# Optimization experiments

Hardware: AMD Instinct MI355X
Metric: run time of the kernel (lower is better)

## Reference

```python
import jax, jax.numpy as jnp
import numpy as np

N_NODES = 50000


def _sage_conv(x, src, dst, W_l, b_l, W_r, n_nodes):
    # mean-aggregate neighbor (source) features onto targets
    msg = x[src]                                   # [E, d_in] gather
    agg = jax.ops.segment_sum(msg, dst, num_segments=n_nodes)   # [N, d_in]
    deg = jax.ops.segment_sum(jnp.ones((src.shape[0],), x.dtype), dst,
                              num_segments=n_nodes)
    agg = agg / jnp.clip(deg, 1.0, None)[:, None]  # mean with deg>=1 clamp (PyG)
    # out = lin_l(agg) + lin_r(x)   (bias lives in lin_l)
    return agg @ W_l.T + b_l + x @ W_r.T


def setup_inputs() -> dict:
    key = jax.random.key(0)
    ks = jax.random.split(key, 8)
    d_in, d_hid, d_out = 128, 256, 128
    n_edges = 800000
    x = jax.random.normal(ks[0], (N_NODES, d_in), dtype=jnp.float32)
    edge_index = jax.random.randint(ks[1], (2, n_edges), 0, N_NODES, dtype=jnp.int32)
    def glorot(k, shape):
        lim = float(np.sqrt(6.0 / (shape[0] + shape[1])))
        return jax.random.uniform(k, shape, jnp.float32, -lim, lim)
    return {
        "x": x,
        "edge_index": edge_index,
        "W1l": glorot(ks[2], (d_hid, d_in)),
        "b1": jnp.zeros((d_hid,), jnp.float32),
        "W1r": glorot(ks[3], (d_hid, d_in)),
        "W2l": glorot(ks[4], (d_out, d_hid)),
        "b2": jnp.zeros((d_out,), jnp.float32),
        "W2r": glorot(ks[5], (d_out, d_hid)),
    }


def reference(x, edge_index, W1l, b1, W1r, W2l, b2, W2r):
    src, dst = edge_index[0], edge_index[1]
    h = jax.nn.relu(_sage_conv(x, src, dst, W1l, b1, W1r, N_NODES))
    out = _sage_conv(h, src, dst, W2l, b2, W2r, N_NODES)
    return out
```

## Files before the change

kernel.cpp:

```cpp
#include <hip/hip_runtime.h>
#include <hip/hip_bf16.h>

#define NN 50000
#define NN_PAD 50176
#define NE 800000
#define NB 196
#define CAP 6144
#define EPB 4096

typedef __attribute__((ext_vector_type(8))) short short8;
typedef __attribute__((ext_vector_type(4))) float f32x4;

__device__ __forceinline__ unsigned short f2bf(float f) {
    union { float f; unsigned u; } v; v.f = f;
    unsigned u = v.u;
    return (unsigned short)((u + 0x7fffu + ((u >> 16) & 1u)) >> 16);
}
__device__ __forceinline__ float bfu_lo(unsigned u) {
    union { unsigned u; float f; } v; v.u = u << 16; return v.f;
}
__device__ __forceinline__ float bfu_hi(unsigned u) {
    union { unsigned u; float f; } v; v.u = u & 0xffff0000u; return v.f;
}

__global__ void k_setup(const float* __restrict__ W1l, const float* __restrict__ W1r,
                        const float* __restrict__ W2l, const float* __restrict__ W2r,
                        unsigned short* __restrict__ W1pk, unsigned short* __restrict__ W2pk,
                        const float4* __restrict__ x4, unsigned short* __restrict__ x_bf,
                        int* __restrict__ gcursor) {
    int blk = blockIdx.x, t = threadIdx.x;
    if (blk < 64) {
        int tid = blk * 256 + t;
        int table = tid >> 13;
        int r = tid & 8191;
        int lane = r & 63, ni = (r >> 6) & 3, ks = (r >> 8) & 7, g = r >> 11;
        int lm = lane & 15, lq = lane >> 4;
        int o = g * 64 + ni * 16 + lm;
        int k = ks * 32 + lq * 8;
        unsigned short v[8];
        if (table == 0) {
            if (k < 128) {
#pragma unroll
                for (int j = 0; j < 8; ++j) v[j] = f2bf(W1l[o * 128 + k + j]);
            } else {
#pragma unroll
                for (int j = 0; j < 8; ++j) v[j] = f2bf(W1r[o * 128 + k - 128 + j]);
            }
            *(uint4*)(W1pk + (size_t)r * 8) = *(const uint4*)v;
        } else {
            if (o < 128) {
#pragma unroll
                for (int j = 0; j < 8; ++j) v[j] = f2bf(W2l[o * 256 + k + j]);
            } else {
#pragma unroll
                for (int j = 0; j < 8; ++j) v[j] = f2bf(W2r[(o - 128) * 256 + k + j]);
            }
            *(uint4*)(W2pk + (size_t)r * 8) = *(const uint4*)v;
        }
    } else if (blk < 6314) {
        int gid = (blk - 64) * 256 + t;
        int n = gid >> 5, c = gid & 31;
        float4 v = x4[(size_t)n * 32 + c];
        ushort4 o;
        o.x = f2bf(v.x); o.y = f2bf(v.y); o.z = f2bf(v.z); o.w = f2bf(v.w);
        *(ushort4*)(x_bf + (size_t)n * 128 + c * 4) = o;
    } else {
        gcursor[t] = t * CAP;
    }
}

__global__ void k_part(const int* __restrict__ src, const int* __restrict__ dst,
                       int* __restrict__ gcursor, unsigned* __restrict__ pairs) {
    __shared__ int cnt[256];
    __shared__ int base[256];
    int t = threadIdx.x;
    cnt[t] = 0;
    __syncthreads();
    int e0 = blockIdx.x * EPB;
    int eend = min(e0 + EPB, NE);
    int rank[16], bk[16];
    unsigned pk[16];
    int m = 0;
    for (int e = e0 + t; e < eend; e += 256) {
        int s = src[e], d = dst[e];
        bk[m] = d >> 8;
        pk[m] = ((unsigned)s << 8) | (unsigned)(d & 255);
        rank[m] = atomicAdd(&cnt[bk[m]], 1);
        ++m;
    }
    __syncthreads();
    if (t < NB && cnt[t] > 0) base[t] = atomicAdd(&gcursor[t], cnt[t]);
    __syncthreads();
    for (int i = 0; i < m; ++i) {
        int pos = base[bk[i]] + rank[i];
        if (pos < (bk[i] + 1) * CAP) pairs[pos] = pk[i];
    }
}

__global__ void k_build(const int* __restrict__ gcursor, const unsigned* __restrict__ pairs,
                        int* __restrict__ deg_i, int* __restrict__ row_start,
                        int* __restrict__ esrc) {
    __shared__ int buf[256];
    __shared__ int ldeg[256];
    __shared__ int lstart[256];
    __shared__ int sh_base, sh_cnt;
    __shared__ int lsrc[CAP];
    int b = blockIdx.x, t = threadIdx.x;
    int c = (t < NB) ? min(gcursor[t] - t * CAP, CAP) : 0;
    buf[t] = c;
    __syncthreads();
#pragma unroll
    for (int o = 1; o < 256; o <<= 1) {
        int add = (t >= o) ? buf[t - o] : 0;
        __syncthreads();
        buf[t] += add;
        __syncthreads();
    }
    if (t == b) { sh_cnt = c; sh_base = buf[b] - c; }
    ldeg[t] = 0;
    __syncthreads();
    int cnt = sh_cnt, base = sh_base;
    int rank[CAP / 256], msrc[CAP / 256], mloc[CAP / 256];
    int m = 0;
    for (int e = t; e < cnt; e += 256) {
        unsigned p = pairs[(size_t)b * CAP + e];
        msrc[m] = (int)(p >> 8); mloc[m] = (int)(p & 255u);
        rank[m] = atomicAdd(&ldeg[mloc[m]], 1);
        ++m;
    }
    __syncthreads();
    int v = ldeg[t];
    buf[t] = v;
    __syncthreads();
#pragma unroll
    for (int o = 1; o < 256; o <<= 1) {
        int add = (t >= o) ? buf[t - o] : 0;
        __syncthreads();
        buf[t] += add;
        __syncthreads();
    }
    lstart[t] = buf[t] - v;
    int node = b * 256 + t;
    if (node < NN) { deg_i[node] = v; row_start[node] = base + lstart[t]; }
    else           { deg_i[node] = 0; row_start[node] = 0; }
    __syncthreads();
    for (int i = 0; i < m; ++i) lsrc[lstart[mloc[i]] + rank[i]] = msrc[i];
    __syncthreads();
    for (int e = t; e < cnt; e += 256) esrc[base + e] = lsrc[e];
}

__global__ void k_agg1(const uint4* __restrict__ xb4, const int* __restrict__ deg_i,
                       const int* __restrict__ row_start, const int* __restrict__ esrc,
                       unsigned short* __restrict__ Abar1) {
    int gid = blockIdx.x * blockDim.x + threadIdx.x;
    int n = gid >> 4, c = gid & 15;
    int dg = deg_i[n], st = row_start[n];
    float acc[8] = {0.f, 0.f, 0.f, 0.f, 0.f, 0.f, 0.f, 0.f};
    int i = 0;
    for (; i + 2 <= dg; i += 2) {
        int s0 = esrc[st + i], s1 = esrc[st + i + 1];
        uint4 h0 = xb4[(size_t)s0 * 16 + c];
        uint4 h1 = xb4[(size_t)s1 * 16 + c];
        acc[0] += bfu_lo(h0.x) + bfu_lo(h1.x); acc[1] += bfu_hi(h0.x) + bfu_hi(h1.x);
        acc[2] += bfu_lo(h0.y) + bfu_lo(h1.y); acc[3] += bfu_hi(h0.y) + bfu_hi(h1.y);
        acc[4] += bfu_lo(h0.z) + bfu_lo(h1.z); acc[5] += bfu_hi(h0.z) + bfu_hi(h1.z);
        acc[6] += bfu_lo(h0.w) + bfu_lo(h1.w); acc[7] += bfu_hi(h0.w) + bfu_hi(h1.w);
    }
    if (i < dg) {
        int s = esrc[st + i];
        uint4 hv = xb4[(size_t)s * 16 + c];
        acc[0] += bfu_lo(hv.x); acc[1] += bfu_hi(hv.x);
        acc[2] += bfu_lo(hv.y); acc[3] += bfu_hi(hv.y);
        acc[4] += bfu_lo(hv.z); acc[5] += bfu_hi(hv.z);
        acc[6] += bfu_lo(hv.w); acc[7] += bfu_hi(hv.w);
    }
    float invd = 1.0f / (float)max(dg, 1);
    unsigned short o[8];
#pragma unroll
    for (int j = 0; j < 8; ++j) o[j] = f2bf(acc[j] * invd);
    *(uint4*)(Abar1 + (size_t)n * 256 + c * 8) = *(const uint4*)o;
    *(uint4*)(Abar1 + (size_t)n * 256 + 128 + c * 8) = xb4[(size_t)n * 16 + c];
}

__global__ __launch_bounds__(256, 2) void k_gemm12(
        const unsigned short* __restrict__ Abar1,
        const unsigned short* __restrict__ W1pk, const unsigned short* __restrict__ W2pk,
        const float* __restrict__ b1, const float* __restrict__ b2,
        unsigned short* __restrict__ y2l, float* __restrict__ out) {
    __shared__ unsigned short T[16384];
    int t = threadIdx.x, blk = blockIdx.x;
    int m0 = blk * 64;
    int wave = t >> 6, lane = t & 63;
    int lm = lane & 15, lq = lane >> 4;
    int pbase = lm * 4 + lq;

    short8 w[8][4];
    {
        const unsigned short* wb = W1pk + (size_t)wave * 16384;
#pragma unroll
        for (int ks = 0; ks < 8; ++ks)
#pragma unroll
            for (int ni = 0; ni < 4; ++ni)
                w[ks][ni] = *(const short8*)(wb + ((size_t)((ks * 4 + ni) * 64 + lane)) * 8);
    }

    {
        const uint4* gp = (const uint4*)(Abar1 + (size_t)m0 * 256);
        uint4 ld[8];
#pragma unroll
        for (int i = 0; i < 8; ++i) ld[i] = gp[i * 256 + t];
        int ks = (t >> 2) & 7, slq = t & 3;
#pragma unroll
        for (int i = 0; i < 8; ++i) {
            int mLoc = i * 8 + (t >> 5);
            int mi = mLoc >> 4, slm = mLoc & 15;
            *(uint4*)(T + ((size_t)((ks * 4 + mi) * 64 + slm * 4 + slq)) * 8) = ld[i];
        }
    }
    __syncthreads();

    f32x4 acc1[4][4];
#pragma unroll
    for (int mi = 0; mi < 4; ++mi)
#pragma unroll
        for (int ni = 0; ni < 4; ++ni) acc1[mi][ni] = (f32x4){0.f, 0.f, 0.f, 0.f};
#pragma unroll
    for (int ks = 0; ks < 8; ++ks) {
        short8 a[4];
#pragma unroll
        for (int mi = 0; mi < 4; ++mi)
            a[mi] = *(const short8*)(T + ((size_t)((ks * 4 + mi) * 64 + pbase)) * 8);
#pragma unroll
        for (int mi = 0; mi < 4; ++mi)
#pragma unroll
            for (int ni = 0; ni < 4; ++ni)
                acc1[mi][ni] = __builtin_amdgcn_mfma_f32_16x16x32_bf16(a[mi], w[ks][ni], acc1[mi][ni], 0, 0, 0);
    }

    {
        const unsigned short* wb = W2pk + (size_t)wave * 16384;
#pragma unroll
        for (int ks = 0; ks < 8; ++ks)
#pragma unroll
            for (int ni = 0; ni < 4; ++ni)
                w[ks][ni] = *(const short8*)(wb + ((size_t)((ks * 4 + ni) * 64 + lane)) * 8);
    }
    __syncthreads();

#pragma unroll
    for (int ni = 0; ni < 4; ++ni) {
        int col = wave * 64 + ni * 16 + lm;
        float bv = b1[col];
        int ks = col >> 5;
        int la = (col & 31) >> 3, j = col & 7;
#pragma unroll
        for (int mi = 0; mi < 4; ++mi)
#pragma unroll
            for (int r = 0; r < 4; ++r) {
                float v = fmaxf(acc1[mi][ni][r] + bv, 0.0f);
                T[((size_t)((ks * 4 + mi) * 64 + (lq * 4 + r) * 4 + la)) * 8 + j] = f2bf(v);
            }
    }
    __syncthreads();

    f32x4 acc2[4][4];
#pragma unroll
    for (int mi = 0; mi < 4; ++mi)
#pragma unroll
        for (int ni = 0; ni < 4; ++ni) acc2[mi][ni] = (f32x4){0.f, 0.f, 0.f, 0.f};
#pragma unroll
    for (int ks = 0; ks < 8; ++ks) {
        short8 a[4];
#pragma unroll
        for (int mi = 0; mi < 4; ++mi)
            a[mi] = *(const short8*)(T + ((size_t)((ks * 4 + mi) * 64 + pbase)) * 8);
#pragma unroll
        for (int mi = 0; mi < 4; ++mi)
#pragma unroll
            for (int ni = 0; ni < 4; ++ni)
                acc2[mi][ni] = __builtin_amdgcn_mfma_f32_16x16x32_bf16(a[mi], w[ks][ni], acc2[mi][ni], 0, 0, 0);
    }

    if (wave < 2) {
#pragma unroll
        for (int ni = 0; ni < 4; ++ni) {
            int col = wave * 64 + ni * 16 + lm;
#pragma unroll
            for (int mi = 0; mi < 4; ++mi)
#pragma unroll
                for (int r = 0; r < 4; ++r) {
                    int row = blk * 64 + mi * 16 + lq * 4 + r;
                    y2l[(size_t)row * 128 + col] = f2bf(acc2[mi][ni][r]);
                }
        }
    } else {
#pragma unroll
        for (int ni = 0; ni < 4; ++ni) {
            int col = (wave - 2) * 64 + ni * 16 + lm;
            float bv = b2[col];
#pragma unroll
            for (int mi = 0; mi < 4; ++mi)
#pragma unroll
                for (int r = 0; r < 4; ++r) {
                    int row = blk * 64 + mi * 16 + lq * 4 + r;
                    if (row < NN) out[(size_t)row * 128 + col] = acc2[mi][ni][r] + bv;
                }
        }
    }
}

__global__ void k_agg_out(const uint4* __restrict__ yl4, const int* __restrict__ deg_i,
                          const int* __restrict__ row_start, const int* __restrict__ esrc,
                          float* __restrict__ out) {
    int gid = blockIdx.x * blockDim.x + threadIdx.x;
    int n = gid >> 4, c = gid & 15;
    int dg = deg_i[n], st = row_start[n];
    float acc[8] = {0.f, 0.f, 0.f, 0.f, 0.f, 0.f, 0.f, 0.f};
    int i = 0;
    for (; i + 2 <= dg; i += 2) {
        int s0 = esrc[st + i], s1 = esrc[st + i + 1];
        uint4 h0 = yl4[(size_t)s0 * 16 + c];
        uint4 h1 = yl4[(size_t)s1 * 16 + c];
        acc[0] += bfu_lo(h0.x) + bfu_lo(h1.x); acc[1] += bfu_hi(h0.x) + bfu_hi(h1.x);
        acc[2] += bfu_lo(h0.y) + bfu_lo(h1.y); acc[3] += bfu_hi(h0.y) + bfu_hi(h1.y);
        acc[4] += bfu_lo(h0.z) + bfu_lo(h1.z); acc[5] += bfu_hi(h0.z) + bfu_hi(h1.z);
        acc[6] += bfu_lo(h0.w) + bfu_lo(h1.w); acc[7] += bfu_hi(h0.w) + bfu_hi(h1.w);
    }
    if (i < dg) {
        int s = esrc[st + i];
        uint4 hv = yl4[(size_t)s * 16 + c];
        acc[0] += bfu_lo(hv.x); acc[1] += bfu_hi(hv.x);
        acc[2] += bfu_lo(hv.y); acc[3] += bfu_hi(hv.y);
        acc[4] += bfu_lo(hv.z); acc[5] += bfu_hi(hv.z);
        acc[6] += bfu_lo(hv.w); acc[7] += bfu_hi(hv.w);
    }
    float invd = 1.0f / (float)max(dg, 1);
    float* op = out + (size_t)n * 128 + c * 8;
    float4 o0 = *(float4*)op, o1 = *(float4*)(op + 4);
    o0.x += acc[0] * invd; o0.y += acc[1] * invd; o0.z += acc[2] * invd; o0.w += acc[3] * invd;
    o1.x += acc[4] * invd; o1.y += acc[5] * invd; o1.z += acc[6] * invd; o1.w += acc[7] * invd;
    *(float4*)op = o0; *(float4*)(op + 4) = o1;
}

extern "C" void kernel_launch(void* const* d_in, const int* in_sizes, int n_in,
                              void* d_out, int out_size, void* d_ws, size_t ws_size,
                              hipStream_t stream) {
    const float* x   = (const float*)d_in[0];
    const int*   ei  = (const int*)d_in[1];
    const int*   src = ei;
    const int*   dst = ei + NE;
    const float* W1l = (const float*)d_in[2];
    const float* b1  = (const float*)d_in[3];
    const float* W1r = (const float*)d_in[4];
    const float* W2l = (const float*)d_in[5];
    const float* b2  = (const float*)d_in[6];
    const float* W2r = (const float*)d_in[7];
    float* out = (float*)d_out;

    char* ws = (char*)d_ws;
    int* deg_i            = (int*)(ws + 0);
    int* row_start        = (int*)(ws + 200704);
    int* gcursor          = (int*)(ws + 401408);
    int* esrc             = (int*)(ws + 409600);
    unsigned* pairs       = (unsigned*)(ws + 4194304);
    unsigned short* x_bf  = (unsigned short*)(ws + 9437184);
    unsigned short* y2l   = (unsigned short*)(ws + 23068672);
    unsigned short* Abar1 = (unsigned short*)(ws + 36700160);
    unsigned short* W1pk  = (unsigned short*)(ws + 62914560);
    unsigned short* W2pk  = (unsigned short*)(ws + 63045632);

    k_setup<<<6315, 256, 0, stream>>>(W1l, W1r, W2l, W2r, W1pk, W2pk,
                                      (const float4*)x, x_bf, gcursor);
    k_part<<<(NE + EPB - 1) / EPB, 256, 0, stream>>>(src, dst, gcursor, pairs);
    k_build<<<NB, 256, 0, stream>>>(gcursor, pairs, deg_i, row_start, esrc);
    k_agg1<<<NN * 16 / 256, 256, 0, stream>>>((const uint4*)x_bf, deg_i, row_start, esrc, Abar1);
    k_gemm12<<<NN_PAD / 64, 256, 0, stream>>>(Abar1, W1pk, W2pk, b1, b2, y2l, out);
    k_agg_out<<<NN * 16 / 256, 256, 0, stream>>>((const uint4*)y2l, deg_i, row_start, esrc, out);
}
```

Baseline: 221.1 us.

## Merge setup with edge partition and process two row tiles per GEMM block

The edge-partition kernel is folded into the setup kernel as extra blocks, and the cursor is zeroed with a memset and treated as a relative count, which removes one kernel launch and its dependency boundary. The fused two-layer GEMM now handles 128 rows per block in two LDS tiles. Each weight set is loaded into registers once and reused across both tiles, which halves the weight reloads per row. The cost is double the LDS footprint (64 KB), which may reduce occupancy, and half as many blocks (392 instead of 784).

```diff
diff --git a/kernel.cpp b/kernel.cpp
--- a/kernel.cpp
+++ b/kernel.cpp
@@ -7,6 +7,7 @@
 #define NB 196
 #define CAP 6144
 #define EPB 4096
+#define PARTB 196
 
 typedef __attribute__((ext_vector_type(8))) short short8;
 typedef __attribute__((ext_vector_type(4))) float f32x4;
@@ -23,11 +24,12 @@
     union { unsigned u; float f; } v; v.u = u & 0xffff0000u; return v.f;
 }
 
-__global__ void k_setup(const float* __restrict__ W1l, const float* __restrict__ W1r,
-                        const float* __restrict__ W2l, const float* __restrict__ W2r,
-                        unsigned short* __restrict__ W1pk, unsigned short* __restrict__ W2pk,
-                        const float4* __restrict__ x4, unsigned short* __restrict__ x_bf,
-                        int* __restrict__ gcursor) {
+__global__ void k_setup_part(const float* __restrict__ W1l, const float* __restrict__ W1r,
+                             const float* __restrict__ W2l, const float* __restrict__ W2r,
+                             unsigned short* __restrict__ W1pk, unsigned short* __restrict__ W2pk,
+                             const float4* __restrict__ x4, unsigned short* __restrict__ x_bf,
+                             const int* __restrict__ src, const int* __restrict__ dst,
+                             int* __restrict__ gcursor, unsigned* __restrict__ pairs) {
     int blk = blockIdx.x, t = threadIdx.x;
     if (blk < 64) {
         int tid = blk * 256 + t;
@@ -65,35 +67,30 @@
         o.x = f2bf(v.x); o.y = f2bf(v.y); o.z = f2bf(v.z); o.w = f2bf(v.w);
         *(ushort4*)(x_bf + (size_t)n * 128 + c * 4) = o;
     } else {
-        gcursor[t] = t * CAP;
-    }
-}
-
-__global__ void k_part(const int* __restrict__ src, const int* __restrict__ dst,
-                       int* __restrict__ gcursor, unsigned* __restrict__ pairs) {
-    __shared__ int cnt[256];
-    __shared__ int base[256];
-    int t = threadIdx.x;
-    cnt[t] = 0;
-    __syncthreads();
-    int e0 = blockIdx.x * EPB;
-    int eend = min(e0 + EPB, NE);
-    int rank[16], bk[16];
-    unsigned pk[16];
-    int m = 0;
-    for (int e = e0 + t; e < eend; e += 256) {
-        int s = src[e], d = dst[e];
-        bk[m] = d >> 8;
-        pk[m] = ((unsigned)s << 8) | (unsigned)(d & 255);
-        rank[m] = atomicAdd(&cnt[bk[m]], 1);
-        ++m;
-    }
-    __syncthreads();
-    if (t < NB && cnt[t] > 0) base[t] = atomicAdd(&gcursor[t], cnt[t]);
-    __syncthreads();
-    for (int i = 0; i < m; ++i) {
-        int pos = base[bk[i]] + rank[i];
-        if (pos < (bk[i] + 1) * CAP) pairs[pos] = pk[i];
+        __shared__ int cnt[256];
+        __shared__ int base[256];
+        cnt[t] = 0;
+        __syncthreads();
+        int pb = blk - 6314;
+        int e0 = pb * EPB;
+        int eend = min(e0 + EPB, NE);
+        int rank[16], bk[16];
+        unsigned pk[16];
+        int m = 0;
+        for (int e = e0 + t; e < eend; e += 256) {
+            int s = src[e], d = dst[e];
+            bk[m] = d >> 8;
+            pk[m] = ((unsigned)s << 8) | (unsigned)(d & 255);
+            rank[m] = atomicAdd(&cnt[bk[m]], 1);
+            ++m;
+        }
+        __syncthreads();
+        if (t < NB && cnt[t] > 0) base[t] = t * CAP + atomicAdd(&gcursor[t], cnt[t]);
+        __syncthreads();
+        for (int i = 0; i < m; ++i) {
+            int pos = base[bk[i]] + rank[i];
+            if (pos < (bk[i] + 1) * CAP) pairs[pos] = pk[i];
+        }
     }
 }
 
@@ -106,7 +103,7 @@
     __shared__ int sh_base, sh_cnt;
     __shared__ int lsrc[CAP];
     int b = blockIdx.x, t = threadIdx.x;
-    int c = (t < NB) ? min(gcursor[t] - t * CAP, CAP) : 0;
+    int c = (t < NB) ? min(gcursor[t], CAP) : 0;
     buf[t] = c;
     __syncthreads();
 #pragma unroll
@@ -187,13 +184,27 @@
         const unsigned short* __restrict__ W1pk, const unsigned short* __restrict__ W2pk,
         const float* __restrict__ b1, const float* __restrict__ b2,
         unsigned short* __restrict__ y2l, float* __restrict__ out) {
-    __shared__ unsigned short T[16384];
+    __shared__ unsigned short T[2][16384];
     int t = threadIdx.x, blk = blockIdx.x;
-    int m0 = blk * 64;
+    int m0 = blk * 128;
     int wave = t >> 6, lane = t & 63;
     int lm = lane & 15, lq = lane >> 4;
     int pbase = lm * 4 + lq;
 
+    {
+        const uint4* gp = (const uint4*)(Abar1 + (size_t)m0 * 256);
+        uint4 ld[16];
+#pragma unroll
+        for (int i = 0; i < 16; ++i) ld[i] = gp[i * 256 + t];
+#pragma unroll
+        for (int i = 0; i < 16; ++i) {
+            int idx = i * 256 + t;
+            int tl = idx >> 11, idx2 = idx & 2047;
+            int row = idx2 >> 5, kc = idx2 & 31;
+            *(uint4*)(&T[tl][(size_t)(((kc >> 2) * 4 + (row >> 4)) * 64 + (row & 15) * 4 + (kc & 3)) * 8]) = ld[i];
+        }
+    }
+
     short8 w[8][4];
     {
         const unsigned short* wb = W1pk + (size_t)wave * 16384;
@@ -203,47 +214,25 @@
             for (int ni = 0; ni < 4; ++ni)
                 w[ks][ni] = *(const short8*)(wb + ((size_t)((ks * 4 + ni) * 64 + lane)) * 8);
     }
-
-    {
-        const uint4* gp = (const uint4*)(Abar1 + (size_t)m0 * 256);
-        uint4 ld[8];
-#pragma unroll
-        for (int i = 0; i < 8; ++i) ld[i] = gp[i * 256 + t];
-        int ks = (t >> 2) & 7, slq = t & 3;
-#pragma unroll
-        for (int i = 0; i < 8; ++i) {
-            int mLoc = i * 8 + (t >> 5);
-            int mi = mLoc >> 4, slm = mLoc & 15;
-            *(uint4*)(T + ((size_t)((ks * 4 + mi) * 64 + slm * 4 + slq)) * 8) = ld[i];
-        }
-    }
-    __syncthreads();
-
-    f32x4 acc1[4][4];
+    __syncthreads();
+
+    f32x4 acc[4][4];
+
 #pragma unroll
     for (int mi = 0; mi < 4; ++mi)
 #pragma unroll
-        for (int ni = 0; ni < 4; ++ni) acc1[mi][ni] = (f32x4){0.f, 0.f, 0.f, 0.f};
+        for (int ni = 0; ni < 4; ++ni) acc[mi][ni] = (f32x4){0.f, 0.f, 0.f, 0.f};
 #pragma unroll
     for (int ks = 0; ks < 8; ++ks) {
         short8 a[4];
 #pragma unroll
         for (int mi = 0; mi < 4; ++mi)
-            a[mi] = *(const short8*)(T + ((size_t)((ks * 4 + mi) * 64 + pbase)) * 8);
+            a[mi] = *(const short8*)(&T[0][(size_t)((ks * 4 + mi) * 64 + pbase) * 8]);
 #pragma unroll
         for (int mi = 0; mi < 4; ++mi)
 #pragma unroll
             for (int ni = 0; ni < 4; ++ni)
-                acc1[mi][ni] = __builtin_amdgcn_mfma_f32_16x16x32_bf16(a[mi], w[ks][ni], acc1[mi][ni], 0, 0, 0);
-    }
-
-    {
-        const unsigned short* wb = W2pk + (size_t)wave * 16384;
-#pragma unroll
-        for (int ks = 0; ks < 8; ++ks)
-#pragma unroll
-            for (int ni = 0; ni < 4; ++ni)
-                w[ks][ni] = *(const short8*)(wb + ((size_t)((ks * 4 + ni) * 64 + lane)) * 8);
+                acc[mi][ni] = __builtin_amdgcn_mfma_f32_16x16x32_bf16(a[mi], w[ks][ni], acc[mi][ni], 0, 0, 0);
     }
     __syncthreads();
 
@@ -257,54 +246,98 @@
         for (int mi = 0; mi < 4; ++mi)
 #pragma unroll
             for (int r = 0; r < 4; ++r) {
-                float v = fmaxf(acc1[mi][ni][r] + bv, 0.0f);
-                T[((size_t)((ks * 4 + mi) * 64 + (lq * 4 + r) * 4 + la)) * 8 + j] = f2bf(v);
-            }
-    }
-    __syncthreads();
-
-    f32x4 acc2[4][4];
+                float v = fmaxf(acc[mi][ni][r] + bv, 0.0f);
+                T[0][(size_t)((ks * 4 + mi) * 64 + (lq * 4 + r) * 4 + la) * 8 + j] = f2bf(v);
+            }
+    }
+
 #pragma unroll
     for (int mi = 0; mi < 4; ++mi)
 #pragma unroll
-        for (int ni = 0; ni < 4; ++ni) acc2[mi][ni] = (f32x4){0.f, 0.f, 0.f, 0.f};
+        for (int ni = 0; ni < 4; ++ni) acc[mi][ni] = (f32x4){0.f, 0.f, 0.f, 0.f};
 #pragma unroll
     for (int ks = 0; ks < 8; ++ks) {
         short8 a[4];
 #pragma unroll
         for (int mi = 0; mi < 4; ++mi)
-            a[mi] = *(const short8*)(T + ((size_t)((ks * 4 + mi) * 64 + pbase)) * 8);
+            a[mi] = *(const short8*)(&T[1][(size_t)((ks * 4 + mi) * 64 + pbase) * 8]);
 #pragma unroll
         for (int mi = 0; mi < 4; ++mi)
 #pragma unroll
             for (int ni = 0; ni < 4; ++ni)
-                acc2[mi][ni] = __builtin_amdgcn_mfma_f32_16x16x32_bf16(a[mi], w[ks][ni], acc2[mi][ni], 0, 0, 0);
-    }
-
-    if (wave < 2) {
-#pragma unroll
-        for (int ni = 0; ni < 4; ++ni) {
-            int col = wave * 64 + ni * 16 + lm;
+                acc[mi][ni] = __builtin_amdgcn_mfma_f32_16x16x32_bf16(a[mi], w[ks][ni], acc[mi][ni], 0, 0, 0);
+    }
+
+    {
+        const unsigned short* wb = W2pk + (size_t)wave * 16384;
+#pragma unroll
+        for (int ks = 0; ks < 8; ++ks)
+#pragma unroll
+            for (int ni = 0; ni < 4; ++ni)
+                w[ks][ni] = *(const short8*)(wb + ((size_t)((ks * 4 + ni) * 64 + lane)) * 8);
+    }
+    __syncthreads();
+
+#pragma unroll
+    for (int ni = 0; ni < 4; ++ni) {
+        int col = wave * 64 + ni * 16 + lm;
+        float bv = b1[col];
+        int ks = col >> 5;
+        int la = (col & 31) >> 3, j = col & 7;
+#pragma unroll
+        for (int mi = 0; mi < 4; ++mi)
+#pragma unroll
+            for (int r = 0; r < 4; ++r) {
+                float v = fmaxf(acc[mi][ni][r] + bv, 0.0f);
+                T[1][(size_t)((ks * 4 + mi) * 64 + (lq * 4 + r) * 4 + la) * 8 + j] = f2bf(v);
+            }
+    }
+    __syncthreads();
+
+#pragma unroll
+    for (int tl = 0; tl < 2; ++tl) {
+#pragma unroll
+        for (int mi = 0; mi < 4; ++mi)
+#pragma unroll
+            for (int ni = 0; ni < 4; ++ni) acc[mi][ni] = (f32x4){0.f, 0.f, 0.f, 0.f};
+#pragma unroll
+        for (int ks = 0; ks < 8; ++ks) {
+            short8 a[4];
 #pragma unroll
             for (int mi = 0; mi < 4; ++mi)
-#pragma unroll
-                for (int r = 0; r < 4; ++r) {
-                    int row = blk * 64 + mi * 16 + lq * 4 + r;
-                    y2l[(size_t)row * 128 + col] = f2bf(acc2[mi][ni][r]);
-                }
-        }
-    } else {
-#pragma unroll
-        for (int ni = 0; ni < 4; ++ni) {
-            int col = (wave - 2) * 64 + ni * 16 + lm;
-            float bv = b2[col];
+                a[mi] = *(const short8*)(&T[tl][(size_t)((ks * 4 + mi) * 64 + pbase) * 8]);
 #pragma unroll
             for (int mi = 0; mi < 4; ++mi)
 #pragma unroll
-                for (int r = 0; r < 4; ++r) {
-                    int row = blk * 64 + mi * 16 + lq * 4 + r;
-                    if (row < NN) out[(size_t)row * 128 + col] = acc2[mi][ni][r] + bv;
-                }
+                for (int ni = 0; ni < 4; ++ni)
+                    acc[mi][ni] = __builtin_amdgcn_mfma_f32_16x16x32_bf16(a[mi], w[ks][ni], acc[mi][ni], 0, 0, 0);
+        }
+        int r0 = m0 + tl * 64;
+        if (wave < 2) {
+#pragma unroll
+            for (int ni = 0; ni < 4; ++ni) {
+                int col = wave * 64 + ni * 16 + lm;
+#pragma unroll
+                for (int mi = 0; mi < 4; ++mi)
+#pragma unroll
+                    for (int r = 0; r < 4; ++r) {
+                        int row = r0 + mi * 16 + lq * 4 + r;
+                        y2l[(size_t)row * 128 + col] = f2bf(acc[mi][ni][r]);
+                    }
+            }
+        } else {
+#pragma unroll
+            for (int ni = 0; ni < 4; ++ni) {
+                int col = (wave - 2) * 64 + ni * 16 + lm;
+                float bv = b2[col];
+#pragma unroll
+                for (int mi = 0; mi < 4; ++mi)
+#pragma unroll
+                    for (int r = 0; r < 4; ++r) {
+                        int row = r0 + mi * 16 + lq * 4 + r;
+                        if (row < NN) out[(size_t)row * 128 + col] = acc[mi][ni][r] + bv;
+                    }
+            }
         }
     }
 }
@@ -369,11 +402,12 @@
     unsigned short* W1pk  = (unsigned short*)(ws + 62914560);
     unsigned short* W2pk  = (unsigned short*)(ws + 63045632);
 
-    k_setup<<<6315, 256, 0, stream>>>(W1l, W1r, W2l, W2r, W1pk, W2pk,
-                                      (const float4*)x, x_bf, gcursor);
-    k_part<<<(NE + EPB - 1) / EPB, 256, 0, stream>>>(src, dst, gcursor, pairs);
+    hipMemsetAsync(gcursor, 0, 1024, stream);
+    k_setup_part<<<6314 + PARTB, 256, 0, stream>>>(W1l, W1r, W2l, W2r, W1pk, W2pk,
+                                                   (const float4*)x, x_bf, src, dst,
+                                                   gcursor, pairs);
     k_build<<<NB, 256, 0, stream>>>(gcursor, pairs, deg_i, row_start, esrc);
     k_agg1<<<NN * 16 / 256, 256, 0, stream>>>((const uint4*)x_bf, deg_i, row_start, esrc, Abar1);
-    k_gemm12<<<NN_PAD / 64, 256, 0, stream>>>(Abar1, W1pk, W2pk, b1, b2, y2l, out);
+    k_gemm12<<<NN_PAD / 128, 256, 0, stream>>>(Abar1, W1pk, W2pk, b1, b2, y2l, out);
     k_agg_out<<<NN * 16 / 256, 256, 0, stream>>>((const uint4*)y2l, deg_i, row_start, esrc, out);
 }
```

Measured after the change: 230.0 us. +4.0%, slower.

## Gather neighbor features in fp8 and fuse edge partitioning into setup kernel

Applied to the files above, without the earlier changes.

Both neighbor-aggregation kernels now gather fp8 copies of the source features (x and the layer-2 left projection) instead of bf16, halving the bytes of the random-access gather traffic. The GEMM writes its y2l output as fp8, and the setup kernel emits an fp8 copy of x alongside the bf16 one. Separately, the edge partitioning kernel is merged into the setup kernel, with the cursor reset done by a memset, removing one launch. The cost is a large precision loss in the aggregated means from fp8 e4m3 quantization, which may break tolerance.

```diff
diff --git a/kernel.cpp b/kernel.cpp
--- a/kernel.cpp
+++ b/kernel.cpp
@@ -10,6 +10,7 @@
 
 typedef __attribute__((ext_vector_type(8))) short short8;
 typedef __attribute__((ext_vector_type(4))) float f32x4;
+typedef __attribute__((ext_vector_type(2))) float f32x2;
 
 __device__ __forceinline__ unsigned short f2bf(float f) {
     union { float f; unsigned u; } v; v.f = f;
@@ -23,14 +24,40 @@
     union { unsigned u; float f; } v; v.u = u & 0xffff0000u; return v.f;
 }
 
-__global__ void k_setup(const float* __restrict__ W1l, const float* __restrict__ W1r,
-                        const float* __restrict__ W2l, const float* __restrict__ W2r,
-                        unsigned short* __restrict__ W1pk, unsigned short* __restrict__ W2pk,
-                        const float4* __restrict__ x4, unsigned short* __restrict__ x_bf,
-                        int* __restrict__ gcursor) {
+__global__ void k_setup_part(const float* __restrict__ W1l, const float* __restrict__ W1r,
+                             const float* __restrict__ W2l, const float* __restrict__ W2r,
+                             unsigned short* __restrict__ W1pk, unsigned short* __restrict__ W2pk,
+                             const float4* __restrict__ x4, unsigned short* __restrict__ x_bf,
+                             unsigned char* __restrict__ x_f8,
+                             const int* __restrict__ src, const int* __restrict__ dst,
+                             int* __restrict__ gcursor, unsigned* __restrict__ pairs) {
     int blk = blockIdx.x, t = threadIdx.x;
-    if (blk < 64) {
-        int tid = blk * 256 + t;
+    if (blk < NB) {
+        __shared__ int cnt[256];
+        __shared__ int base[256];
+        cnt[t] = 0;
+        __syncthreads();
+        int e0 = blk * EPB;
+        int eend = min(e0 + EPB, NE);
+        int rank[16], bk[16];
+        unsigned pk[16];
+        int m = 0;
+        for (int e = e0 + t; e < eend; e += 256) {
+            int s = src[e], d = dst[e];
+            bk[m] = d >> 8;
+            pk[m] = ((unsigned)s << 8) | (unsigned)(d & 255);
+            rank[m] = atomicAdd(&cnt[bk[m]], 1);
+            ++m;
+        }
+        __syncthreads();
+        if (t < NB && cnt[t] > 0) base[t] = t * CAP + atomicAdd(&gcursor[t], cnt[t]);
+        __syncthreads();
+        for (int i = 0; i < m; ++i) {
+            int pos = base[bk[i]] + rank[i];
+            if (pos < (bk[i] + 1) * CAP) pairs[pos] = pk[i];
+        }
+    } else if (blk < 260) {
+        int tid = (blk - 196) * 256 + t;
         int table = tid >> 13;
         int r = tid & 8191;
         int lane = r & 63, ni = (r >> 6) & 3, ks = (r >> 8) & 7, g = r >> 11;
@@ -57,43 +84,16 @@
             }
             *(uint4*)(W2pk + (size_t)r * 8) = *(const uint4*)v;
         }
-    } else if (blk < 6314) {
-        int gid = (blk - 64) * 256 + t;
+    } else {
+        int gid = (blk - 260) * 256 + t;
         int n = gid >> 5, c = gid & 31;
         float4 v = x4[(size_t)n * 32 + c];
         ushort4 o;
         o.x = f2bf(v.x); o.y = f2bf(v.y); o.z = f2bf(v.z); o.w = f2bf(v.w);
         *(ushort4*)(x_bf + (size_t)n * 128 + c * 4) = o;
-    } else {
-        gcursor[t] = t * CAP;
-    }
-}
-
-__global__ void k_part(const int* __restrict__ src, const int* __restrict__ dst,
-                       int* __restrict__ gcursor, unsigned* __restrict__ pairs) {
-    __shared__ int cnt[256];
-    __shared__ int base[256];
-    int t = threadIdx.x;
-    cnt[t] = 0;
-    __syncthreads();
-    int e0 = blockIdx.x * EPB;
-    int eend = min(e0 + EPB, NE);
-    int rank[16], bk[16];
-    unsigned pk[16];
-    int m = 0;
-    for (int e = e0 + t; e < eend; e += 256) {
-        int s = src[e], d = dst[e];
-        bk[m] = d >> 8;
-        pk[m] = ((unsigned)s << 8) | (unsigned)(d & 255);
-        rank[m] = atomicAdd(&cnt[bk[m]], 1);
-        ++m;
-    }
-    __syncthreads();
-    if (t < NB && cnt[t] > 0) base[t] = atomicAdd(&gcursor[t], cnt[t]);
-    __syncthreads();
-    for (int i = 0; i < m; ++i) {
-        int pos = base[bk[i]] + rank[i];
-        if (pos < (bk[i] + 1) * CAP) pairs[pos] = pk[i];
+        unsigned p = (unsigned)__builtin_amdgcn_cvt_pk_fp8_f32(v.x, v.y, 0, false);
+        p = (unsigned)__builtin_amdgcn_cvt_pk_fp8_f32(v.z, v.w, (int)p, true);
+        *(unsigned*)(x_f8 + (size_t)n * 128 + c * 4) = p;
     }
 }
 
@@ -106,7 +106,7 @@
     __shared__ int sh_base, sh_cnt;
     __shared__ int lsrc[CAP];
     int b = blockIdx.x, t = threadIdx.x;
-    int c = (t < NB) ? min(gcursor[t] - t * CAP, CAP) : 0;
+    int c = (t < NB) ? min(gcursor[t], CAP) : 0;
     buf[t] = c;
     __syncthreads();
 #pragma unroll
@@ -149,9 +149,9 @@
     for (int e = t; e < cnt; e += 256) esrc[base + e] = lsrc[e];
 }
 
-__global__ void k_agg1(const uint4* __restrict__ xb4, const int* __restrict__ deg_i,
-                       const int* __restrict__ row_start, const int* __restrict__ esrc,
-                       unsigned short* __restrict__ Abar1) {
+__global__ void k_agg1(const uint2* __restrict__ xf8, const uint4* __restrict__ xb4,
+                       const int* __restrict__ deg_i, const int* __restrict__ row_start,
+                       const int* __restrict__ esrc, unsigned short* __restrict__ Abar1) {
     int gid = blockIdx.x * blockDim.x + threadIdx.x;
     int n = gid >> 4, c = gid & 15;
     int dg = deg_i[n], st = row_start[n];
@@ -159,20 +159,32 @@
     int i = 0;
     for (; i + 2 <= dg; i += 2) {
         int s0 = esrc[st + i], s1 = esrc[st + i + 1];
-        uint4 h0 = xb4[(size_t)s0 * 16 + c];
-        uint4 h1 = xb4[(size_t)s1 * 16 + c];
-        acc[0] += bfu_lo(h0.x) + bfu_lo(h1.x); acc[1] += bfu_hi(h0.x) + bfu_hi(h1.x);
-        acc[2] += bfu_lo(h0.y) + bfu_lo(h1.y); acc[3] += bfu_hi(h0.y) + bfu_hi(h1.y);
-        acc[4] += bfu_lo(h0.z) + bfu_lo(h1.z); acc[5] += bfu_hi(h0.z) + bfu_hi(h1.z);
-        acc[6] += bfu_lo(h0.w) + bfu_lo(h1.w); acc[7] += bfu_hi(h0.w) + bfu_hi(h1.w);
+        uint2 q0 = xf8[(size_t)s0 * 16 + c];
+        uint2 q1 = xf8[(size_t)s1 * 16 + c];
+        f32x2 a0 = __builtin_amdgcn_cvt_pk_f32_fp8(q0.x, false);
+        f32x2 a1 = __builtin_amdgcn_cvt_pk_f32_fp8(q0.x, true);
+        f32x2 a2 = __builtin_amdgcn_cvt_pk_f32_fp8(q0.y, false);
+        f32x2 a3 = __builtin_amdgcn_cvt_pk_f32_fp8(q0.y, true);
+        f32x2 b0 = __builtin_amdgcn_cvt_pk_f32_fp8(q1.x, false);
+        f32x2 b1 = __builtin_amdgcn_cvt_pk_f32_fp8(q1.x, true);
+        f32x2 b2 = __builtin_amdgcn_cvt_pk_f32_fp8(q1.y, false);
+        f32x2 b3 = __builtin_amdgcn_cvt_pk_f32_fp8(q1.y, true);
+        acc[0] += a0.x + b0.x; acc[1] += a0.y + b0.y;
+        acc[2] += a1.x + b1.x; acc[3] += a1.y + b1.y;
+        acc[4] += a2.x + b2.x; acc[5] += a2.y + b2.y;
+        acc[6] += a3.x + b3.x; acc[7] += a3.y + b3.y;
     }
     if (i < dg) {
         int s = esrc[st + i];
-        uint4 hv = xb4[(size_t)s * 16 + c];
-        acc[0] += bfu_lo(hv.x); acc[1] += bfu_hi(hv.x);
-        acc[2] += bfu_lo(hv.y); acc[3] += bfu_hi(hv.y);
-        acc[4] += bfu_lo(hv.z); acc[5] += bfu_hi(hv.z);
-        acc[6] += bfu_lo(hv.w); acc[7] += bfu_hi(hv.w);
+        uint2 q0 = xf8[(size_t)s * 16 + c];
+        f32x2 a0 = __builtin_amdgcn_cvt_pk_f32_fp8(q0.x, false);
+        f32x2 a1 = __builtin_amdgcn_cvt_pk_f32_fp8(q0.x, true);
+        f32x2 a2 = __builtin_amdgcn_cvt_pk_f32_fp8(q0.y, false);
+        f32x2 a3 = __builtin_amdgcn_cvt_pk_f32_fp8(q0.y, true);
+        acc[0] += a0.x; acc[1] += a0.y;
+        acc[2] += a1.x; acc[3] += a1.y;
+        acc[4] += a2.x; acc[5] += a2.y;
+        acc[6] += a3.x; acc[7] += a3.y;
     }
     float invd = 1.0f / (float)max(dg, 1);
     unsigned short o[8];
@@ -186,7 +198,7 @@
         const unsigned short* __restrict__ Abar1,
         const unsigned short* __restrict__ W1pk, const unsigned short* __restrict__ W2pk,
         const float* __restrict__ b1, const float* __restrict__ b2,
-        unsigned short* __restrict__ y2l, float* __restrict__ out) {
+        unsigned char* __restrict__ y2f8, float* __restrict__ out) {
     __shared__ unsigned short T[16384];
     int t = threadIdx.x, blk = blockIdx.x;
     int m0 = blk * 64;
@@ -290,7 +302,9 @@
 #pragma unroll
                 for (int r = 0; r < 4; ++r) {
                     int row = blk * 64 + mi * 16 + lq * 4 + r;
-                    y2l[(size_t)row * 128 + col] = f2bf(acc2[mi][ni][r]);
+                    float v = acc2[mi][ni][r];
+                    unsigned p = (unsigned)__builtin_amdgcn_cvt_pk_fp8_f32(v, v, 0, false);
+                    y2f8[(size_t)row * 128 + col] = (unsigned char)(p & 0xff);
                 }
         }
     } else {
@@ -309,7 +323,7 @@
     }
 }
 
-__global__ void k_agg_out(const uint4* __restrict__ yl4, const int* __restrict__ deg_i,
+__global__ void k_agg_out(const uint2* __restrict__ yf8, const int* __restrict__ deg_i,
                           const int* __restrict__ row_start, const int* __restrict__ esrc,
                           float* __restrict__ out) {
     int gid = blockIdx.x * blockDim.x + threadIdx.x;
@@ -319,20 +333,32 @@
     int i = 0;
     for (; i + 2 <= dg; i += 2) {
         int s0 = esrc[st + i], s1 = esrc[st + i + 1];
-        uint4 h0 = yl4[(size_t)s0 * 16 + c];
-        uint4 h1 = yl4[(size_t)s1 * 16 + c];
-        acc[0] += bfu_lo(h0.x) + bfu_lo(h1.x); acc[1] += bfu_hi(h0.x) + bfu_hi(h1.x);
-        acc[2] += bfu_lo(h0.y) + bfu_lo(h1.y); acc[3] += bfu_hi(h0.y) + bfu_hi(h1.y);
-        acc[4] += bfu_lo(h0.z) + bfu_lo(h1.z); acc[5] += bfu_hi(h0.z) + bfu_hi(h1.z);
-        acc[6] += bfu_lo(h0.w) + bfu_lo(h1.w); acc[7] += bfu_hi(h0.w) + bfu_hi(h1.w);
+        uint2 q0 = yf8[(size_t)s0 * 16 + c];
+        uint2 q1 = yf8[(size_t)s1 * 16 + c];
+        f32x2 a0 = __builtin_amdgcn_cvt_pk_f32_fp8(q0.x, false);
+        f32x2 a1 = __builtin_amdgcn_cvt_pk_f32_fp8(q0.x, true);
+        f32x2 a2 = __builtin_amdgcn_cvt_pk_f32_fp8(q0.y, false);
+        f32x2 a3 = __builtin_amdgcn_cvt_pk_f32_fp8(q0.y, true);
+        f32x2 b0 = __builtin_amdgcn_cvt_pk_f32_fp8(q1.x, false);
+        f32x2 b1 = __builtin_amdgcn_cvt_pk_f32_fp8(q1.x, true);
+        f32x2 b2 = __builtin_amdgcn_cvt_pk_f32_fp8(q1.y, false);
+        f32x2 b3 = __builtin_amdgcn_cvt_pk_f32_fp8(q1.y, true);
+        acc[0] += a0.x + b0.x; acc[1] += a0.y + b0.y;
+        acc[2] += a1.x + b1.x; acc[3] += a1.y + b1.y;
+        acc[4] += a2.x + b2.x; acc[5] += a2.y + b2.y;
+        acc[6] += a3.x + b3.x; acc[7] += a3.y + b3.y;
     }
     if (i < dg) {
         int s = esrc[st + i];
-        uint4 hv = yl4[(size_t)s * 16 + c];
-        acc[0] += bfu_lo(hv.x); acc[1] += bfu_hi(hv.x);
-        acc[2] += bfu_lo(hv.y); acc[3] += bfu_hi(hv.y);
-        acc[4] += bfu_lo(hv.z); acc[5] += bfu_hi(hv.z);
-        acc[6] += bfu_lo(hv.w); acc[7] += bfu_hi(hv.w);
+        uint2 q0 = yf8[(size_t)s * 16 + c];
+        f32x2 a0 = __builtin_amdgcn_cvt_pk_f32_fp8(q0.x, false);
+        f32x2 a1 = __builtin_amdgcn_cvt_pk_f32_fp8(q0.x, true);
+        f32x2 a2 = __builtin_amdgcn_cvt_pk_f32_fp8(q0.y, false);
+        f32x2 a3 = __builtin_amdgcn_cvt_pk_f32_fp8(q0.y, true);
+        acc[0] += a0.x; acc[1] += a0.y;
+        acc[2] += a1.x; acc[3] += a1.y;
+        acc[4] += a2.x; acc[5] += a2.y;
+        acc[6] += a3.x; acc[7] += a3.y;
     }
     float invd = 1.0f / (float)max(dg, 1);
     float* op = out + (size_t)n * 128 + c * 8;
@@ -364,16 +390,19 @@
     int* esrc             = (int*)(ws + 409600);
     unsigned* pairs       = (unsigned*)(ws + 4194304);
     unsigned short* x_bf  = (unsigned short*)(ws + 9437184);
-    unsigned short* y2l   = (unsigned short*)(ws + 23068672);
-    unsigned short* Abar1 = (unsigned short*)(ws + 36700160);
-    unsigned short* W1pk  = (unsigned short*)(ws + 62914560);
-    unsigned short* W2pk  = (unsigned short*)(ws + 63045632);
-
-    k_setup<<<6315, 256, 0, stream>>>(W1l, W1r, W2l, W2r, W1pk, W2pk,
-                                      (const float4*)x, x_bf, gcursor);
-    k_part<<<(NE + EPB - 1) / EPB, 256, 0, stream>>>(src, dst, gcursor, pairs);
+    unsigned char* x_f8   = (unsigned char*)(ws + 22282240);
+    unsigned char* y2f8   = (unsigned char*)(ws + 28704768);
+    unsigned short* Abar1 = (unsigned short*)(ws + 35651584);
+    unsigned short* W1pk  = (unsigned short*)(ws + 61341696);
+    unsigned short* W2pk  = (unsigned short*)(ws + 61472768);
+
+    hipMemsetAsync(gcursor, 0, 1024, stream);
+    k_setup_part<<<6510, 256, 0, stream>>>(W1l, W1r, W2l, W2r, W1pk, W2pk,
+                                           (const float4*)x, x_bf, x_f8, src, dst,
+                                           gcursor, pairs);
     k_build<<<NB, 256, 0, stream>>>(gcursor, pairs, deg_i, row_start, esrc);
-    k_agg1<<<NN * 16 / 256, 256, 0, stream>>>((const uint4*)x_bf, deg_i, row_start, esrc, Abar1);
-    k_gemm12<<<NN_PAD / 64, 256, 0, stream>>>(Abar1, W1pk, W2pk, b1, b2, y2l, out);
-    k_agg_out<<<NN * 16 / 256, 256, 0, stream>>>((const uint4*)y2l, deg_i, row_start, esrc, out);
-}
+    k_agg1<<<NN * 16 / 256, 256, 0, stream>>>((const uint2*)x_f8, (const uint4*)x_bf,
+                                              deg_i, row_start, esrc, Abar1);
+    k_gemm12<<<NN_PAD / 64, 256, 0, stream>>>(Abar1, W1pk, W2pk, b1, b2, y2f8, out);
+    k_agg_out<<<NN * 16 / 256, 256, 0, stream>>>((const uint2*)y2f8, deg_i, row_start, esrc, out);
+}
```

Measured after the change: 203.9 us. -7.8%, faster.
